# Performance work log

Measured on AMD Instinct MI355X. Metric: run time of the kernel, lower is better.

Reference implementation:

```python
import jax, jax.numpy as jnp
import numpy as np

B, S, D, V = 4, 1024, 512, 8192
SCALES = [1, 2, 4, 8, 16]   # nn.Parameter init; used via int(scale.item()) -> static
WIN = 8                     # min(8, S//2) in compute_semantic_coherence
EPS = 1e-5


def layer_norm(x, g, b):
    m = x.mean(-1, keepdims=True)
    v = ((x - m) ** 2).mean(-1, keepdims=True)
    return (x - m) / jnp.sqrt(v + EPS) * g + b


def setup_inputs() -> dict:
    key = jax.random.key(0)
    ks = jax.random.split(key, 24)
    n = lambda k, shape, s=0.02: (jax.random.normal(k, shape, jnp.float32) * s)
    return {
        "embeddings": jax.random.normal(ks[0], (B, S, D), jnp.float32),
        "token_ids": jax.random.randint(ks[1], (B, S), 0, V),
        "context_mask": jnp.ones((B, S), jnp.float32),
        "token_similarity": n(ks[2], (V, V)),
        "W_scale": n(ks[3], (len(SCALES), D), 0.05), "b_scale": jnp.zeros((D,), jnp.float32),
        "W_sem": n(ks[4], (1, D), 0.05), "b_sem": jnp.zeros((D,), jnp.float32),
        "W_ctx": n(ks[5], (D, D), 0.02), "b_ctx": jnp.zeros((D,), jnp.float32),
        "W_fuse": n(ks[6], (4 * D, D), 0.02), "b_fuse": jnp.zeros((D,), jnp.float32),
        "ln1_g": jnp.ones((D,), jnp.float32), "ln1_b": jnp.zeros((D,), jnp.float32),
        "ln2_g": jnp.ones((D,), jnp.float32), "ln2_b": jnp.zeros((D,), jnp.float32),
        "ln3_g": jnp.ones((D,), jnp.float32), "ln3_b": jnp.zeros((D,), jnp.float32),
        "W_e0": n(ks[7], (D, D), 0.02), "b_e0": jnp.zeros((D,), jnp.float32),
        "W_e1": n(ks[8], (D, D), 0.02), "b_e1": jnp.zeros((D,), jnp.float32),
        "W_e2": n(ks[9], (D, D), 0.02), "b_e2": jnp.zeros((D,), jnp.float32),
    }


def _forward(embeddings, token_ids, context_mask, token_similarity,
             W_scale, b_scale, W_sem, b_sem, W_ctx, b_ctx, W_fuse, b_fuse,
             ln1_g, ln1_b, ln2_g, ln2_b, ln3_g, ln3_b,
             W_e0, b_e0, W_e1, b_e1, W_e2, b_e2):
    phases = jnp.tanh(embeddings)  # [B,S,D]

    # --- multi-scale coherence via cumulative sums + cos angle-difference identity ---
    # mean_t cos(p_t - m) = cos(m)*mean(cos p) + sin(m)*mean(sin p) over each window
    z = jnp.zeros((B, 1, D), phases.dtype)
    cum_p = jnp.concatenate([z, jnp.cumsum(phases, 1)], 1)            # [B,S+1,D]
    cum_c = jnp.concatenate([z, jnp.cumsum(jnp.cos(phases), 1)], 1)
    cum_s = jnp.concatenate([z, jnp.cumsum(jnp.sin(phases), 1)], 1)
    cols = []
    for s in SCALES:
        wm = (cum_p[:, s:] - cum_p[:, :-s]) / s   # window mean  [B,S-s+1,D]
        ac = (cum_c[:, s:] - cum_c[:, :-s]) / s   # window mean cos
        asn = (cum_s[:, s:] - cum_s[:, :-s]) / s  # window mean sin
        coh = jnp.mean(jnp.cos(wm) * ac + jnp.sin(wm) * asn, -1)      # [B,S-s+1]
        cols.append(jnp.pad(coh, ((0, 0), (0, s - 1))))               # torch leaves tail zeros
    msc = jnp.stack(cols, -1)                                         # [B,S,num_scales]
    scale_coh = msc @ W_scale + b_scale                               # [B,S,D]

    # --- semantic coherence (windowed, sim-weighted; torch takes mean over WHOLE tensor incl. batch) ---
    te = token_similarity[token_ids]                                  # [B,S,V]
    ten = te / jnp.maximum(jnp.linalg.norm(te, axis=-1, keepdims=True), 1e-12)
    tsim = jnp.einsum('biv,bjv->bij', ten, ten)                       # [B,S,S]
    off = jnp.arange(-WIN, WIN + 1)
    pos = jnp.arange(S)[:, None] + off[None, :]                       # [S,17]
    valid = (pos >= 0) & (pos < S)
    posc = jnp.clip(pos, 0, S - 1)
    pwin = phases[:, posc]                                            # [B,S,17,D]
    swin = jnp.take_along_axis(tsim, jnp.broadcast_to(posc[None], (B, S, 2 * WIN + 1)), axis=2)
    coh = jnp.cos((phases[:, :, None, :] - pwin) * swin[..., None]) * valid[None, :, :, None].astype(phases.dtype)
    counts = valid.sum(1).astype(phases.dtype)                        # [S]
    sem = coh.sum((0, 2, 3)) / (B * counts * D)                       # [S] (same scalar for all batches)
    sem = jnp.broadcast_to(sem[None, :], (B, S))[..., None]           # [B,S,1]
    sem_coh = sem @ W_sem + b_sem                                     # [B,S,D]

    # --- context coherence (context_mask path) ---
    cmean = jnp.mean(embeddings * context_mask[..., None], 1, keepdims=True)
    ctx_coh = jnp.cos(embeddings - cmean) @ W_ctx + b_ctx

    # --- local coherence ---
    lc = jnp.cos(embeddings[:, 1:] - embeddings[:, :-1])
    lc = jnp.concatenate([lc, jnp.zeros((B, 1, D), embeddings.dtype)], 1)

    allc = jnp.concatenate([scale_coh, sem_coh, ctx_coh, lc], -1)     # [B,S,4D]
    x = layer_norm(allc @ W_fuse + b_fuse, ln1_g, ln1_b)
    x = jax.nn.gelu(x, approximate=False)                             # dropout = identity (eval)
    for W, bb in ((W_e0, b_e0), (W_e1, b_e1), (W_e2, b_e2)):
        r = x
        h = layer_norm(x, ln2_g, ln2_b) @ W + bb
        x = r + jax.nn.gelu(h, approximate=False) * 0.1
    return layer_norm(x, ln3_g, ln3_b)


def reference(embeddings, token_ids, context_mask, token_similarity,
              W_scale, b_scale, W_sem, b_sem, W_ctx, b_ctx, W_fuse, b_fuse,
              ln1_g, ln1_b, ln2_g, ln2_b, ln3_g, ln3_b,
              W_e0, b_e0, W_e1, b_e1, W_e2, b_e2):
    return _forward(embeddings, token_ids, context_mask, token_similarity,
                    W_scale, b_scale, W_sem, b_sem, W_ctx, b_ctx, W_fuse, b_fuse,
                    ln1_g, ln1_b, ln2_g, ln2_b, ln3_g, ln3_b,
                    W_e0, b_e0, W_e1, b_e1, W_e2, b_e2)
```

## Files before the change

kernel.cpp:

```cpp
#include <hip/hip_runtime.h>


#define DEV __device__ __forceinline__
typedef unsigned short u16;
typedef __bf16 bf16x8 __attribute__((ext_vector_type(8)));
typedef float f32x4 __attribute__((ext_vector_type(4)));

static constexpr int S = 1024;
static constexpr int D = 512;
static constexpr int KCAT = 1056;

DEV u16 f2bf(float f) {
  unsigned u = __float_as_uint(f);
  return (u16)((u + 0x7fffu + ((u >> 16) & 1u)) >> 16);
}
DEV float gelu(float x) { return 0.5f * x * (1.f + erff(x * 0.70710678118654752f)); }
DEV float wred(float v) {
#pragma unroll
  for (int off = 32; off; off >>= 1) v += __shfl_down(v, off, 64);
  return v;
}
DEV void bred2(float& a, float& b, float* sm, int tid) {
  a = wred(a); b = wred(b);
  int w = tid >> 6;
  if ((tid & 63) == 0) { sm[w] = a; sm[w + 4] = b; }
  __syncthreads();
  a = sm[0] + sm[1] + sm[2] + sm[3];
  b = sm[4] + sm[5] + sm[6] + sm[7];
  __syncthreads();
}
DEV float qred(float v) {
  v += __shfl_xor(v, 1, 64);
  v += __shfl_xor(v, 2, 64);
  return v;
}

__global__ __launch_bounds__(256) void k_pre(const float* __restrict__ emb,
                                             const float* __restrict__ mask,
                                             float* __restrict__ ph,
                                             float* __restrict__ cmacc) {
  int blk = blockIdx.x, tid = threadIdx.x;
  if (blk < 1024) {
    int idx = blk * 256 + tid;
#pragma unroll
    for (int r = 0; r < 2; ++r, idx += 262144) {
      float4 v = ((const float4*)emb)[idx];
      float4 o;
      o.x = tanhf(v.x); o.y = tanhf(v.y); o.z = tanhf(v.z); o.w = tanhf(v.w);
      ((float4*)ph)[idx] = o;
    }
  } else {
    int r = blk - 1024, b = r >> 3, chunk = r & 7;
    float a0 = 0.f, a1 = 0.f;
    for (int s = chunk * 128; s < chunk * 128 + 128; ++s) {
      float m = mask[b * S + s];
      const float* row = emb + (size_t)(b * S + s) * D;
      a0 += row[tid] * m; a1 += row[tid + 256] * m;
    }
    atomicAdd(cmacc + b * D + tid, a0);
    atomicAdd(cmacc + b * D + tid + 256, a1);
  }
}

static constexpr int CP = 129;
__global__ __launch_bounds__(256) void k_dots(const float* __restrict__ sim,
                                              const int* __restrict__ tok,
                                              float* __restrict__ dots_raw,
                                              float* __restrict__ normsq) {
  __shared__ float sT[72 * CP];
  __shared__ int stok[72];
  int bx = blockIdx.x, cy = blockIdx.y, tid = threadIdx.x;
  int b = bx >> 4, g0 = (bx & 15) * 64, gidx = b * S + g0;
  if (tid < 72) {
    int p = g0 + tid;
    stok[tid] = (p < S) ? tok[b * S + p] : -1;
  }
  __syncthreads();
  const float4* sim4 = (const float4*)sim;
#pragma unroll
  for (int it = 0; it < 9; ++it) {
    int u = it * 256 + tid, r = u >> 5, q = u & 31;
    int tk = stok[r];
    float4 v = make_float4(0.f, 0.f, 0.f, 0.f);
    if (tk >= 0) v = sim4[(size_t)tk * 2048 + cy * 32 + q];
    float* dst = &sT[r * CP + 4 * q];
    dst[0] = v.x; dst[1] = v.y; dst[2] = v.z; dst[3] = v.w;
  }
  __syncthreads();
  int wave = tid >> 6, lane = tid & 63;
  float acc[9] = {};
  const float* base = &sT[lane * CP + wave * 32];
#pragma unroll 4
  for (int cc = 0; cc < 32; ++cc) {
    float va = base[cc];
    acc[8] += va * va;
#pragma unroll
    for (int o = 1; o <= 8; ++o) acc[o - 1] += va * base[o * CP + cc];
  }
  __syncthreads();
  float* red = sT;
#pragma unroll
  for (int s = 0; s < 9; ++s) red[(wave * 9 + s) * 64 + lane] = acc[s];
  __syncthreads();
  for (int u = tid; u < 576; u += 256) {
    int s = u >> 6, a = u & 63;
    float v = red[s * 64 + a] + red[(9 + s) * 64 + a] +
              red[(18 + s) * 64 + a] + red[(27 + s) * 64 + a];
    if (s < 8) atomicAdd(&dots_raw[(size_t)(gidx + a) * 8 + s], v);
    else       atomicAdd(&normsq[gidx + a], v);
  }
}

static constexpr int CP2 = 132;
__global__ __launch_bounds__(256) void k_coh(const float* __restrict__ ph,
                                             const float* __restrict__ dots_raw,
                                             const float* __restrict__ normsq,
                                             float* __restrict__ msc_raw,
                                             float* __restrict__ semacc) {
  __shared__ float sP[88 * CP2];
  __shared__ float sw2[64 * 17];
  int bx = blockIdx.x, dy = blockIdx.y, tid = threadIdx.x;
  int b = bx >> 4, g0 = (bx & 15) * 64;
  const float4* ph4 = (const float4*)ph;
#pragma unroll
  for (int it = 0; it < 11; ++it) {
    int u = it * 256 + tid, r = u >> 5, q = u & 31;
    int gr = g0 - 8 + r;
    gr = gr < 0 ? 0 : (gr > S - 1 ? S - 1 : gr);
    float4 v = ph4[(size_t)(b * S + gr) * 128 + dy * 32 + q];
    *(float4*)&sP[r * CP2 + 4 * q] = v;
  }
  for (int u = tid; u < 1088; u += 256) {
    int a = u / 17, oi = u - a * 17;
    int i = g0 + a, o = oi - 8, j = i + o;
    int idx = b * S + i;
    float v = 0.f;
    if (j >= 0 && j < S) {
      if (o == 0) v = 1.f;
      else {
        float dr = (o > 0) ? dots_raw[(size_t)idx * 8 + o - 1]
                           : dots_raw[(size_t)(idx + o) * 8 + (-o - 1)];
        float ni = fmaxf(sqrtf(normsq[idx]), 1e-12f);
        float nj = fmaxf(sqrtf(normsq[idx + o]), 1e-12f);
        v = dr / (ni * nj);
      }
    }
    sw2[u] = v;
  }
  __syncthreads();
  int ar = tid >> 2, dq = tid & 3;
  int i = g0 + ar, idx = b * S + i;
  int jmax = S - 1 - i; if (jmax > 15) jmax = 15;
  float swr[17];
#pragma unroll
  for (int oi = 0; oi < 17; ++oi) swr[oi] = sw2[ar * 17 + oi];
  float a0 = 0.f, a1 = 0.f, a2 = 0.f, a3 = 0.f, a4 = 0.f, asem = 0.f;
#pragma unroll 2
  for (int dd = 0; dd < 32; ++dd) {
    int d = dq + 4 * dd;
    const float* pb = &sP[(ar + 8) * CP2 + d];
    float sp = 0.f, sc = 0.f, ss = 0.f;
#pragma unroll
    for (int j = 0; j < 16; ++j) {
      float x = (j <= jmax) ? pb[j * CP2] : 0.f;
      sp += x; sc += __cosf(x); ss += __sinf(x);
      if (j == 0) a0 += __cosf(sp) * sc + __sinf(sp) * ss;
      else if (j == 1)  { float wm = sp * 0.5f;    a1 += __cosf(wm) * (sc * 0.5f)    + __sinf(wm) * (ss * 0.5f); }
      else if (j == 3)  { float wm = sp * 0.25f;   a2 += __cosf(wm) * (sc * 0.25f)   + __sinf(wm) * (ss * 0.25f); }
      else if (j == 7)  { float wm = sp * 0.125f;  a3 += __cosf(wm) * (sc * 0.125f)  + __sinf(wm) * (ss * 0.125f); }
      else if (j == 15) { float wm = sp * 0.0625f; a4 += __cosf(wm) * (sc * 0.0625f) + __sinf(wm) * (ss * 0.0625f); }
    }
    float p0 = pb[0];
    const float* qb = &sP[ar * CP2 + d];
#pragma unroll
    for (int oi = 0; oi < 17; ++oi) {
      int j = i + oi - 8;
      bool valid = (j >= 0) && (j < S);
      float pj = qb[oi * CP2];
      asem += valid ? __cosf((p0 - pj) * swr[oi]) : 0.f;
    }
  }
  a0 = qred(a0); a1 = qred(a1); a2 = qred(a2); a3 = qred(a3); a4 = qred(a4);
  asem = qred(asem);
  if (dq == 0) {
    float* mr = msc_raw + (size_t)idx * 5;
    atomicAdd(mr + 0, a0); atomicAdd(mr + 1, a1); atomicAdd(mr + 2, a2);
    atomicAdd(mr + 3, a3); atomicAdd(mr + 4, a4);
    atomicAdd(semacc + i, asem);
  }
}

__global__ __launch_bounds__(256) void k_wbig(const float* __restrict__ W0,
    const float* __restrict__ W1, const float* __restrict__ W2,
    const float* __restrict__ Wf, const float* __restrict__ wctx,
    const float* __restrict__ Wsc, const float* __restrict__ Wsm,
    const float* __restrict__ bsc, const float* __restrict__ bsm,
    const float* __restrict__ bcx,
    u16* __restrict__ T0, u16* __restrict__ T1, u16* __restrict__ T2,
    u16* __restrict__ wcatT, float* __restrict__ ctx_acc,
    float* __restrict__ sm_acc) {
  __shared__ float tile[64][65];
  int blk = blockIdx.x, tid = threadIdx.x;
  if (blk < 256) {
    int z = blk >> 6, rem = blk & 63;
    const float* src = z == 0 ? W0 : z == 1 ? W1 : z == 2 ? W2 : Wf + (size_t)1536 * 512;
    int r0 = (rem >> 3) * 64, c0 = (rem & 7) * 64;
    int tr = tid >> 6, tc = tid & 63;
#pragma unroll 4
    for (int i = 0; i < 16; ++i)
      tile[tr + i * 4][tc] = src[(size_t)(r0 + tr + i * 4) * 512 + c0 + tc];
    __syncthreads();
#pragma unroll 4
    for (int i = 0; i < 16; ++i) {
      int n = c0 + tr + i * 4, k = r0 + tc;
      u16 v = f2bf(tile[tc][tr + i * 4]);
      if (z == 3) wcatT[(size_t)n * KCAT + 512 + k] = v;
      else (z == 0 ? T0 : z == 1 ? T1 : T2)[(size_t)n * 512 + k] = v;
    }
  } else if (blk < 512) {
    int rem = blk - 256;
    int n = (rem & 1) * 256 + tid;
    int kbase = ((rem & 63) >> 1) * 16;
    int j0 = (rem >> 6) * 128;
    float acc[16] = {};
    for (int j = j0; j < j0 + 128; ++j) {
      float wf3 = Wf[(size_t)(1024 + j) * 512 + n];
#pragma unroll
      for (int kk = 0; kk < 16; ++kk) acc[kk] += wctx[(size_t)(kbase + kk) * 512 + j] * wf3;
    }
#pragma unroll
    for (int kk = 0; kk < 16; ++kk)
      atomicAdd(&ctx_acc[(size_t)(kbase + kk) * 512 + n], acc[kk]);
  } else {
    int rem = blk - 512;
    int n = (rem & 1) * 256 + tid;
    int j0 = (rem >> 1) * 16;
    float a0 = 0.f, a1 = 0.f, a2 = 0.f, a3 = 0.f, a4 = 0.f, au = 0.f, ac = 0.f;
    for (int j = j0; j < j0 + 16; ++j) {
      float wf1 = Wf[(size_t)j * 512 + n];
      float wf2 = Wf[(size_t)(512 + j) * 512 + n];
      float wf3 = Wf[(size_t)(1024 + j) * 512 + n];
      a0 += Wsc[j] * wf1; a1 += Wsc[512 + j] * wf1; a2 += Wsc[1024 + j] * wf1;
      a3 += Wsc[1536 + j] * wf1; a4 += Wsc[2048 + j] * wf1;
      au += Wsm[j] * wf2;
      ac += bsc[j] * wf1 + bsm[j] * wf2 + bcx[j] * wf3;
    }
    atomicAdd(&sm_acc[0 * 512 + n], a0);
    atomicAdd(&sm_acc[1 * 512 + n], a1);
    atomicAdd(&sm_acc[2 * 512 + n], a2);
    atomicAdd(&sm_acc[3 * 512 + n], a3);
    atomicAdd(&sm_acc[4 * 512 + n], a4);
    atomicAdd(&sm_acc[5 * 512 + n], au);
    atomicAdd(&sm_acc[6 * 512 + n], ac);
  }
}

__global__ __launch_bounds__(256) void k_packfin(const float* __restrict__ ctx_acc,
    const float* __restrict__ sm_acc, const float* __restrict__ bfu,
    u16* __restrict__ wcatT) {
  __shared__ float tile[64][65];
  int blk = blockIdx.x, tid = threadIdx.x;
  if (blk < 64) {
    int r0 = (blk >> 3) * 64, c0 = (blk & 7) * 64;
    int tr = tid >> 6, tc = tid & 63;
#pragma unroll 4
    for (int i = 0; i < 16; ++i)
      tile[tr + i * 4][tc] = ctx_acc[(size_t)(r0 + tr + i * 4) * 512 + c0 + tc];
    __syncthreads();
#pragma unroll 4
    for (int i = 0; i < 16; ++i)
      wcatT[(size_t)(c0 + tr + i * 4) * KCAT + r0 + tc] = f2bf(tile[tc][tr + i * 4]);
  } else {
    int n = (blk - 64) * 256 + tid;
    u16* row = wcatT + (size_t)n * KCAT;
#pragma unroll
    for (int s = 0; s < 6; ++s) row[1024 + s] = f2bf(sm_acc[s * 512 + n]);
    row[1030] = f2bf(sm_acc[6 * 512 + n] + bfu[n]);
    for (int k = 1031; k < KCAT; ++k) row[k] = 0;
  }
}

__global__ __launch_bounds__(256) void k_xcat(const float* __restrict__ emb,
    const float* __restrict__ cmacc, const float* __restrict__ msc_raw,
    const float* __restrict__ semacc, u16* __restrict__ xcat) {
  int idx = blockIdx.x, b = idx >> 10, i = idx & 1023, tid = threadIdx.x;
  const float* erow = emb + (size_t)idx * D;
  u16* orow = xcat + (size_t)idx * KCAT;
  for (int c = tid; c < KCAT; c += 256) {
    float v;
    if (c < 512) {
      v = __cosf(erow[c] - cmacc[b * D + c] * (1.f / 1024.f));
    } else if (c < 1024) {
      int d = c - 512;
      v = (i < S - 1) ? __cosf(erow[D + d] - erow[d]) : 0.f;
    } else if (c < 1029) {
      int s = c - 1024, req = (1 << s) - 1;
      v = (S - 1 - i >= req) ? msc_raw[(size_t)idx * 5 + s] * (1.f / 512.f) : 0.f;
    } else if (c == 1029) {
      int cnt = ((i < 8) ? i : 8) + ((S - 1 - i < 8) ? (S - 1 - i) : 8) + 1;
      v = semacc[i] / (4.f * (float)cnt * 512.f);
    } else if (c == 1030) {
      v = 1.f;
    } else v = 0.f;
    orow[c] = f2bf(v);
  }
}

__global__ __launch_bounds__(256) void k_gemm(const u16* __restrict__ A,
    const u16* __restrict__ BT, float* __restrict__ C,
    const float* __restrict__ bias, int K) {
  __shared__ __align__(16) u16 sA[64 * 40];
  __shared__ __align__(16) u16 sB[64 * 40];
  int tid = threadIdx.x, wave = tid >> 6, lane = tid & 63;
  int m0 = blockIdx.x * 64, n0 = blockIdx.y * 64;
  int lr = tid >> 2, lc = (tid & 3) * 8;
  int q8 = (lane >> 4) * 8, l15 = lane & 15;
  const u16* Ap = A + (size_t)(m0 + lr) * K + lc;
  const u16* Bp = BT + (size_t)(n0 + lr) * K + lc;
  f32x4 acc[4] = {};
  for (int k0 = 0; k0 < K; k0 += 32) {
    *(uint4*)&sA[lr * 40 + lc] = *(const uint4*)(Ap + k0);
    *(uint4*)&sB[lr * 40 + lc] = *(const uint4*)(Bp + k0);
    __syncthreads();
    bf16x8 af = *(const bf16x8*)&sA[(wave * 16 + l15) * 40 + q8];
#pragma unroll
    for (int f = 0; f < 4; ++f) {
      bf16x8 bfr = *(const bf16x8*)&sB[(f * 16 + l15) * 40 + q8];
      acc[f] = __builtin_amdgcn_mfma_f32_16x16x32_bf16(af, bfr, acc[f], 0, 0, 0);
    }
    __syncthreads();
  }
  int r0 = m0 + wave * 16 + (lane >> 4) * 4;
#pragma unroll
  for (int f = 0; f < 4; ++f) {
    int col = n0 + f * 16 + l15;
    float bv = bias ? bias[col] : 0.f;
#pragma unroll
    for (int r = 0; r < 4; ++r)
      C[(size_t)(r0 + r) * 512 + col] = acc[f][r] + bv;
  }
}

__global__ __launch_bounds__(256) void k_post_y1(const float* __restrict__ y,
    float* __restrict__ x, u16* __restrict__ t,
    const float* __restrict__ g1, const float* __restrict__ b1,
    const float* __restrict__ g2, const float* __restrict__ b2) {
  __shared__ float sm[8];
  int row = blockIdx.x, tid = threadIdx.x;
  size_t base = (size_t)row * 512;
  float v0 = y[base + tid], v1 = y[base + tid + 256];
  float s = v0 + v1, ss = v0 * v0 + v1 * v1;
  bred2(s, ss, sm, tid);
  float m = s * (1.f / 512.f);
  float inv = rsqrtf(ss * (1.f / 512.f) - m * m + 1e-5f);
  float x0 = gelu((v0 - m) * inv * g1[tid] + b1[tid]);
  float x1 = gelu((v1 - m) * inv * g1[tid + 256] + b1[tid + 256]);
  x[base + tid] = x0; x[base + tid + 256] = x1;
  s = x0 + x1; ss = x0 * x0 + x1 * x1;
  bred2(s, ss, sm, tid);
  m = s * (1.f / 512.f);
  inv = rsqrtf(ss * (1.f / 512.f) - m * m + 1e-5f);
  t[base + tid] = f2bf((x0 - m) * inv * g2[tid] + b2[tid]);
  t[base + tid + 256] = f2bf((x1 - m) * inv * g2[tid + 256] + b2[tid + 256]);
}

__global__ __launch_bounds__(256) void k_post_res(const float* __restrict__ h,
    float* __restrict__ x, u16* __restrict__ t, float* __restrict__ out,
    const float* __restrict__ g, const float* __restrict__ bb, int final_) {
  __shared__ float sm[8];
  int row = blockIdx.x, tid = threadIdx.x;
  size_t base = (size_t)row * 512;
  float x0 = x[base + tid] + 0.1f * gelu(h[base + tid]);
  float x1 = x[base + tid + 256] + 0.1f * gelu(h[base + tid + 256]);
  float s = x0 + x1, ss = x0 * x0 + x1 * x1;
  bred2(s, ss, sm, tid);
  float m = s * (1.f / 512.f);
  float inv = rsqrtf(ss * (1.f / 512.f) - m * m + 1e-5f);
  float n0 = (x0 - m) * inv * g[tid] + bb[tid];
  float n1 = (x1 - m) * inv * g[tid + 256] + bb[tid + 256];
  if (final_) {
    out[base + tid] = n0; out[base + tid + 256] = n1;
  } else {
    x[base + tid] = x0; x[base + tid + 256] = x1;
    t[base + tid] = f2bf(n0); t[base + tid + 256] = f2bf(n1);
  }
}

extern "C" void kernel_launch(void* const* d_in, const int* in_sizes, int n_in,
                              void* d_out, int out_size, void* d_ws, size_t ws_size,
                              hipStream_t stream) {
  const float* emb     = (const float*)d_in[0];
  const int*   tok     = (const int*)d_in[1];
  const float* mask    = (const float*)d_in[2];
  const float* sim     = (const float*)d_in[3];
  const float* W_scale = (const float*)d_in[4];
  const float* b_scale = (const float*)d_in[5];
  const float* W_sem   = (const float*)d_in[6];
  const float* b_sem   = (const float*)d_in[7];
  const float* W_ctx   = (const float*)d_in[8];
  const float* b_ctx   = (const float*)d_in[9];
  const float* W_fuse  = (const float*)d_in[10];
  const float* b_fuse  = (const float*)d_in[11];
  const float* ln1_g = (const float*)d_in[12], *ln1_b = (const float*)d_in[13];
  const float* ln2_g = (const float*)d_in[14], *ln2_b = (const float*)d_in[15];
  const float* ln3_g = (const float*)d_in[16], *ln3_b = (const float*)d_in[17];
  const float* W_e0 = (const float*)d_in[18], *b_e0 = (const float*)d_in[19];
  const float* W_e1 = (const float*)d_in[20], *b_e1 = (const float*)d_in[21];
  const float* W_e2 = (const float*)d_in[22], *b_e2 = (const float*)d_in[23];
  float* out = (float*)d_out;

  char* w = (char*)d_ws; size_t off = 0;
  auto alloc = [&](size_t bytes) { void* p = w + off; off += (bytes + 255) & ~(size_t)255; return p; };
  float* phases = (float*)alloc((size_t)4096 * 512 * 4);
  float* hbuf   = (float*)alloc((size_t)4096 * 512 * 4);
  float* xbuf   = (float*)alloc((size_t)4096 * 512 * 4);
  u16*   tbuf   = (u16*)  alloc((size_t)4096 * 512 * 2);
  u16*   xcat   = (u16*)  alloc((size_t)4096 * KCAT * 2);
  u16*   wcatT  = (u16*)  alloc((size_t)512 * KCAT * 2);
  u16*   We0T   = (u16*)  alloc((size_t)512 * 512 * 2);
  u16*   We1T   = (u16*)  alloc((size_t)512 * 512 * 2);
  u16*   We2T   = (u16*)  alloc((size_t)512 * 512 * 2);
  float* semacc   = (float*)alloc((size_t)1024 * 4);
  float* cmacc    = (float*)alloc((size_t)4 * 512 * 4);
  float* dots_raw = (float*)alloc((size_t)4096 * 8 * 4);
  float* normsq   = (float*)alloc((size_t)4096 * 4);
  float* msc_raw  = (float*)alloc((size_t)4096 * 5 * 4);
  float* ctx_acc  = (float*)alloc((size_t)512 * 512 * 4);
  float* sm_acc   = (float*)alloc((size_t)7 * 512 * 4);
  (void)ws_size; (void)in_sizes; (void)n_in; (void)out_size;

  size_t zbytes = (size_t)(1024 + 4 * 512 + 4096 * 8 + 4096 + 4096 * 5 + 512 * 512 + 7 * 512) * 4;
  hipMemsetAsync(semacc, 0, zbytes, stream);

  k_pre<<<1056, 256, 0, stream>>>(emb, mask, phases, cmacc);
  k_dots<<<dim3(64, 64), 256, 0, stream>>>(sim, tok, dots_raw, normsq);
  k_coh<<<dim3(64, 4), 256, 0, stream>>>(phases, dots_raw, normsq, msc_raw, semacc);

  k_wbig<<<576, 256, 0, stream>>>(W_e0, W_e1, W_e2, W_fuse, W_ctx,
                                  W_scale, W_sem, b_scale, b_sem, b_ctx,
                                  We0T, We1T, We2T, wcatT, ctx_acc, sm_acc);
  k_packfin<<<66, 256, 0, stream>>>(ctx_acc, sm_acc, b_fuse, wcatT);

  k_xcat<<<4096, 256, 0, stream>>>(emb, cmacc, msc_raw, semacc, xcat);
  k_gemm<<<dim3(64, 8), 256, 0, stream>>>(xcat, wcatT, hbuf, nullptr, KCAT);
  k_post_y1<<<4096, 256, 0, stream>>>(hbuf, xbuf, tbuf, ln1_g, ln1_b, ln2_g, ln2_b);

  k_gemm<<<dim3(64, 8), 256, 0, stream>>>(tbuf, We0T, hbuf, b_e0, 512);
  k_post_res<<<4096, 256, 0, stream>>>(hbuf, xbuf, tbuf, nullptr, ln2_g, ln2_b, 0);
  k_gemm<<<dim3(64, 8), 256, 0, stream>>>(tbuf, We1T, hbuf, b_e1, 512);
  k_post_res<<<4096, 256, 0, stream>>>(hbuf, xbuf, tbuf, nullptr, ln2_g, ln2_b, 0);
  k_gemm<<<dim3(64, 8), 256, 0, stream>>>(tbuf, We2T, hbuf, b_e2, 512);
  k_post_res<<<4096, 256, 0, stream>>>(hbuf, xbuf, nullptr, out, ln3_g, ln3_b, 1);
}
```

Measured before the change: 610.9 us.

## Vectorize dots LDS reads, halve coh D-tile, double GEMM K-step

k_dots now uses float4 LDS stores and f32x4 reads with vector accumulators, padding rows to 132 floats for alignment. k_coh splits D into 8 slices of 64 instead of 4 of 128, doubling the grid for more parallelism on a launch that had only 256 blocks. k_gemm now stages 64 K-elements per sync instead of 32, halving barriers per tile, and KCAT is raised to 1088 so it divides by 64. Risks: the KCAT change must match how xcat and wcatT are packed and zero-padded, and k_coh's halo reloads and per-block overhead double.

```diff
diff --git a/kernel.cpp b/kernel.cpp
--- a/kernel.cpp
+++ b/kernel.cpp
@@ -8,7 +8,7 @@
 
 static constexpr int S = 1024;
 static constexpr int D = 512;
-static constexpr int KCAT = 1056;
+static constexpr int KCAT = 1088;
 
 DEV u16 f2bf(float f) {
   unsigned u = __float_as_uint(f);
@@ -62,12 +62,12 @@
   }
 }
 
-static constexpr int CP = 129;
+static constexpr int CP = 132;
 __global__ __launch_bounds__(256) void k_dots(const float* __restrict__ sim,
                                               const int* __restrict__ tok,
                                               float* __restrict__ dots_raw,
                                               float* __restrict__ normsq) {
-  __shared__ float sT[72 * CP];
+  __shared__ __align__(16) float sT[72 * CP];
   __shared__ int stok[72];
   int bx = blockIdx.x, cy = blockIdx.y, tid = threadIdx.x;
   int b = bx >> 4, g0 = (bx & 15) * 64, gidx = b * S + g0;
@@ -83,24 +83,29 @@
     int tk = stok[r];
     float4 v = make_float4(0.f, 0.f, 0.f, 0.f);
     if (tk >= 0) v = sim4[(size_t)tk * 2048 + cy * 32 + q];
-    float* dst = &sT[r * CP + 4 * q];
-    dst[0] = v.x; dst[1] = v.y; dst[2] = v.z; dst[3] = v.w;
+    *(float4*)&sT[r * CP + 4 * q] = v;
   }
   __syncthreads();
   int wave = tid >> 6, lane = tid & 63;
-  float acc[9] = {};
+  f32x4 acc[9] = {};
   const float* base = &sT[lane * CP + wave * 32];
-#pragma unroll 4
-  for (int cc = 0; cc < 32; ++cc) {
-    float va = base[cc];
+#pragma unroll 2
+  for (int c4 = 0; c4 < 8; ++c4) {
+    f32x4 va = *(const f32x4*)(base + 4 * c4);
     acc[8] += va * va;
 #pragma unroll
-    for (int o = 1; o <= 8; ++o) acc[o - 1] += va * base[o * CP + cc];
+    for (int o = 1; o <= 8; ++o) {
+      f32x4 vb = *(const f32x4*)(base + o * CP + 4 * c4);
+      acc[o - 1] += va * vb;
+    }
   }
   __syncthreads();
   float* red = sT;
 #pragma unroll
-  for (int s = 0; s < 9; ++s) red[(wave * 9 + s) * 64 + lane] = acc[s];
+  for (int s = 0; s < 9; ++s) {
+    f32x4 a = acc[s];
+    red[(wave * 9 + s) * 64 + lane] = a[0] + a[1] + a[2] + a[3];
+  }
   __syncthreads();
   for (int u = tid; u < 576; u += 256) {
     int s = u >> 6, a = u & 63;
@@ -111,24 +116,27 @@
   }
 }
 
-static constexpr int CP2 = 132;
+static constexpr int CP2 = 68;
 __global__ __launch_bounds__(256) void k_coh(const float* __restrict__ ph,
                                              const float* __restrict__ dots_raw,
                                              const float* __restrict__ normsq,
                                              float* __restrict__ msc_raw,
                                              float* __restrict__ semacc) {
-  __shared__ float sP[88 * CP2];
+  __shared__ __align__(16) float sP[88 * CP2];
   __shared__ float sw2[64 * 17];
   int bx = blockIdx.x, dy = blockIdx.y, tid = threadIdx.x;
   int b = bx >> 4, g0 = (bx & 15) * 64;
   const float4* ph4 = (const float4*)ph;
 #pragma unroll
-  for (int it = 0; it < 11; ++it) {
-    int u = it * 256 + tid, r = u >> 5, q = u & 31;
-    int gr = g0 - 8 + r;
-    gr = gr < 0 ? 0 : (gr > S - 1 ? S - 1 : gr);
-    float4 v = ph4[(size_t)(b * S + gr) * 128 + dy * 32 + q];
-    *(float4*)&sP[r * CP2 + 4 * q] = v;
+  for (int it = 0; it < 6; ++it) {
+    int u = it * 256 + tid;
+    if (u < 1408) {
+      int r = u >> 4, q = u & 15;
+      int gr = g0 - 8 + r;
+      gr = gr < 0 ? 0 : (gr > S - 1 ? S - 1 : gr);
+      float4 v = ph4[(size_t)(b * S + gr) * 128 + dy * 16 + q];
+      *(float4*)&sP[r * CP2 + 4 * q] = v;
+    }
   }
   for (int u = tid; u < 1088; u += 256) {
     int a = u / 17, oi = u - a * 17;
@@ -156,7 +164,7 @@
   for (int oi = 0; oi < 17; ++oi) swr[oi] = sw2[ar * 17 + oi];
   float a0 = 0.f, a1 = 0.f, a2 = 0.f, a3 = 0.f, a4 = 0.f, asem = 0.f;
 #pragma unroll 2
-  for (int dd = 0; dd < 32; ++dd) {
+  for (int dd = 0; dd < 16; ++dd) {
     int d = dq + 4 * dd;
     const float* pb = &sP[(ar + 8) * CP2 + d];
     float sp = 0.f, sc = 0.f, ss = 0.f;
@@ -309,8 +317,8 @@
 __global__ __launch_bounds__(256) void k_gemm(const u16* __restrict__ A,
     const u16* __restrict__ BT, float* __restrict__ C,
     const float* __restrict__ bias, int K) {
-  __shared__ __align__(16) u16 sA[64 * 40];
-  __shared__ __align__(16) u16 sB[64 * 40];
+  __shared__ __align__(16) u16 sA[64 * 72];
+  __shared__ __align__(16) u16 sB[64 * 72];
   int tid = threadIdx.x, wave = tid >> 6, lane = tid & 63;
   int m0 = blockIdx.x * 64, n0 = blockIdx.y * 64;
   int lr = tid >> 2, lc = (tid & 3) * 8;
@@ -318,15 +326,21 @@
   const u16* Ap = A + (size_t)(m0 + lr) * K + lc;
   const u16* Bp = BT + (size_t)(n0 + lr) * K + lc;
   f32x4 acc[4] = {};
-  for (int k0 = 0; k0 < K; k0 += 32) {
-    *(uint4*)&sA[lr * 40 + lc] = *(const uint4*)(Ap + k0);
-    *(uint4*)&sB[lr * 40 + lc] = *(const uint4*)(Bp + k0);
+  for (int k0 = 0; k0 < K; k0 += 64) {
+    *(uint4*)&sA[lr * 72 + lc]      = *(const uint4*)(Ap + k0);
+    *(uint4*)&sA[lr * 72 + lc + 32] = *(const uint4*)(Ap + k0 + 32);
+    *(uint4*)&sB[lr * 72 + lc]      = *(const uint4*)(Bp + k0);
+    *(uint4*)&sB[lr * 72 + lc + 32] = *(const uint4*)(Bp + k0 + 32);
     __syncthreads();
-    bf16x8 af = *(const bf16x8*)&sA[(wave * 16 + l15) * 40 + q8];
+    int row = wave * 16 + l15;
+    bf16x8 af0 = *(const bf16x8*)&sA[row * 72 + q8];
+    bf16x8 af1 = *(const bf16x8*)&sA[row * 72 + 32 + q8];
 #pragma unroll
     for (int f = 0; f < 4; ++f) {
-      bf16x8 bfr = *(const bf16x8*)&sB[(f * 16 + l15) * 40 + q8];
-      acc[f] = __builtin_amdgcn_mfma_f32_16x16x32_bf16(af, bfr, acc[f], 0, 0, 0);
+      bf16x8 b0 = *(const bf16x8*)&sB[(f * 16 + l15) * 72 + q8];
+      bf16x8 b1 = *(const bf16x8*)&sB[(f * 16 + l15) * 72 + 32 + q8];
+      acc[f] = __builtin_amdgcn_mfma_f32_16x16x32_bf16(af0, b0, acc[f], 0, 0, 0);
+      acc[f] = __builtin_amdgcn_mfma_f32_16x16x32_bf16(af1, b1, acc[f], 0, 0, 0);
     }
     __syncthreads();
   }
@@ -434,7 +448,7 @@
 
   k_pre<<<1056, 256, 0, stream>>>(emb, mask, phases, cmacc);
   k_dots<<<dim3(64, 64), 256, 0, stream>>>(sim, tok, dots_raw, normsq);
-  k_coh<<<dim3(64, 4), 256, 0, stream>>>(phases, dots_raw, normsq, msc_raw, semacc);
+  k_coh<<<dim3(64, 8), 256, 0, stream>>>(phases, dots_raw, normsq, msc_raw, semacc);
 
   k_wbig<<<576, 256, 0, stream>>>(W_e0, W_e1, W_e2, W_fuse, W_ctx,
                                   W_scale, W_sem, b_scale, b_sem, b_ctx,
```

New measurement: 591.7 us. 1.03x faster.
